# Performance work log

Measured on AMD Instinct MI355X. Metric: run time of the kernel, lower is better.

The kernel has to match this reference:

```python
import jax, jax.numpy as jnp
import numpy as np
import math

B, LQ, LK = 1024, 1, 1024
LQD, SQD, H = 256, 128, 2
HD = SQD // H  # 64
EPS = 1e-6


def _ln(x, g, b):
    mu = x.mean(-1, keepdims=True)
    var = ((x - mu) ** 2).mean(-1, keepdims=True)
    return (x - mu) / jnp.sqrt(var + EPS) * g + b


def setup_inputs() -> dict:
    key = jax.random.key(0)
    ks = jax.random.split(key, 16)
    w = lambda k, s: jax.random.normal(k, s, jnp.float32) * 0.02
    return {
        "q_feats": jax.random.normal(ks[0], (B, LQ, LQD), jnp.float32),
        "k_feats": jax.random.normal(ks[1], (B, LK, SQD), jnp.float32),
        "msk": jax.random.randint(ks[2], (B, LK), 0, 2).astype(jnp.int32),
        "ln1_g": jnp.ones(LQD), "ln1_b": jnp.zeros(LQD),
        "W1": w(ks[3], (LQD, SQD)), "b1": jnp.zeros(SQD),
        "lnq_g": jnp.ones(SQD), "lnq_b": jnp.zeros(SQD),
        "lnk_g": jnp.ones(SQD), "lnk_b": jnp.zeros(SQD),
        "Wq": w(ks[4], (SQD, SQD)), "bq": jnp.zeros(SQD),
        "Wk": w(ks[5], (SQD, SQD)), "bk": jnp.zeros(SQD),
        "Wv": w(ks[6], (SQD, SQD)), "bv": jnp.zeros(SQD),
        "Wo": w(ks[7], (SQD, SQD)), "bo": jnp.zeros(SQD),
        "scale_w": jax.random.uniform(ks[8], (SQD,), jnp.float32, 0.01, 2.0),
        "ln2_g": jnp.ones(SQD), "ln2_b": jnp.zeros(SQD),
        "W2": w(ks[9], (SQD, LQD)), "b2": jnp.zeros(LQD),
    }


def reference(q_feats, k_feats, msk, ln1_g, ln1_b, W1, b1, lnq_g, lnq_b,
              lnk_g, lnk_b, Wq, bq, Wk, bk, Wv, bv, Wo, bo, scale_w,
              ln2_g, ln2_b, W2, b2):
    gelu = lambda x: jax.nn.gelu(x, approximate=False)
    # q_block1: LN -> Linear -> GELU (dropout = identity in eval)
    q_atten = gelu(_ln(q_feats, ln1_g, ln1_b) @ W1 + b1)  # [B,LQ,SQD]
    kv_in = _ln(k_feats, lnk_g, lnk_b)                     # [B,LK,SQD]
    q_in = _ln(q_atten, lnq_g, lnq_b)
    # masked self-attention
    qh = (q_in @ Wq + bq).reshape(B, LQ, H, HD).transpose(0, 2, 1, 3)
    kh = (kv_in @ Wk + bk).reshape(B, LK, H, HD).transpose(0, 2, 1, 3)
    vh = (kv_in @ Wv + bv).reshape(B, LK, H, HD).transpose(0, 2, 1, 3)
    scores = jnp.einsum('bhqd,bhkd->bhqk', qh, kh) / math.sqrt(HD)
    m = msk.astype(scores.dtype)[:, None, None, :]  # [B,1,1,LK]
    scores = jnp.where(m == 0, -1e9, scores * m)
    attn = jax.nn.softmax(scores, axis=-1)
    ctx = jnp.einsum('bhqk,bhkd->bhqd', attn, vh)
    ctx = ctx.transpose(0, 2, 1, 3).reshape(B, LQ, SQD)
    attn_out = gelu(ctx @ Wo + bo)
    q_atten = q_atten + attn_out
    # scaled broadcast residual into k_feats
    scaled = jnp.swapaxes(q_atten * scale_w, 0, 1)         # [LQ,B,SQD]
    k_out = k_feats + jnp.tile(scaled, (B, 1, 1))          # [B,B,SQD]
    # q_block2
    q_out = q_feats + gelu(_ln(q_atten, ln2_g, ln2_b) @ W2 + b2)
    return (q_out, k_out)
```

## Files before the change

kernel.cpp:

```cpp
#include <hip/hip_runtime.h>
#include <math.h>

#define B_    1024
#define LK_   1024
#define LQD_  256
#define SQD_  128
#define EPSLN 1e-6f
#define LOG2E 1.4426950408889634f

#define TROWS 16
#define TF4   33
#define WREGF4 (TROWS * TF4)
#define WREGF  (WREGF4 * 4)

typedef float floatx4 __attribute__((ext_vector_type(4)));

__device__ __forceinline__ float gelu_exact(float x) {
    return 0.5f * x * (1.0f + erff(x * 0.70710678118654752f));
}

__global__ __launch_bounds__(256, 4)
void fused_joint_kernel(
    const float* __restrict__ q_feats, const float* __restrict__ k_feats,
    const int*   __restrict__ msk,
    const float* __restrict__ ln1_g, const float* __restrict__ ln1_b,
    const float* __restrict__ W1,    const float* __restrict__ b1,
    const float* __restrict__ lnq_g, const float* __restrict__ lnq_b,
    const float* __restrict__ lnk_g, const float* __restrict__ lnk_b,
    const float* __restrict__ Wq,    const float* __restrict__ bq,
    const float* __restrict__ Wk,    const float* __restrict__ bk,
    const float* __restrict__ Wv,    const float* __restrict__ bv,
    const float* __restrict__ Wo,    const float* __restrict__ bo,
    const float* __restrict__ scale_w,
    const float* __restrict__ ln2_g, const float* __restrict__ ln2_b,
    const float* __restrict__ W2,    const float* __restrict__ b2,
    float* __restrict__ q_out, float* __restrict__ k_out)
{
    const int b    = blockIdx.x;
    const int tid  = threadIdx.x;
    const int wave = tid >> 6;
    const int lane = tid & 63;

    __shared__ float4 s_tile4[4 * WREGF4];
    __shared__ float4 s_meta[4][TROWS];
    __shared__ unsigned short s_idxm[4][256];
    __shared__ __align__(16) float s_gu[2][128];
    __shared__ float s_q1[128];
    __shared__ float s_sc[128];
    __shared__ float s_red[8];
    __shared__ float s_ml[4][2][2];

    float* s_flat = (float*)s_tile4;
    float* s_qn = s_flat;
    float* s_qi = s_flat + 256;
    float* s_qh = s_flat + 384;
    float* s_u0 = s_flat + 512;
    float* s_u1 = s_flat + 640;
    float* s_c2 = s_flat + 768;
    float* s_wn  = s_flat + 1024;
    float* s_ctx = s_flat + 1280;
    float* s_qa  = s_flat + 1408;
    float* s_qn2 = s_flat + 1536;

    float x = q_feats[b * LQD_ + tid];
    float rs = x, rss = x * x;
    #pragma unroll
    for (int o = 32; o >= 1; o >>= 1) { rs += __shfl_xor(rs, o); rss += __shfl_xor(rss, o); }
    if (lane == 0) { s_red[wave * 2] = rs; s_red[wave * 2 + 1] = rss; }
    __syncthreads();
    {
        float sum  = s_red[0] + s_red[2] + s_red[4] + s_red[6];
        float ssum = s_red[1] + s_red[3] + s_red[5] + s_red[7];
        float mu   = sum * (1.0f / 256.0f);
        float var  = ssum * (1.0f / 256.0f) - mu * mu;
        float rstd = rsqrtf(var + EPSLN);
        s_qn[tid] = (x - mu) * rstd * ln1_g[tid] + ln1_b[tid];
    }
    __syncthreads();

    if (tid < 128) {
        float acc = b1[tid];
        #pragma unroll 4
        for (int c = 0; c < 256; ++c) acc = fmaf(s_qn[c], W1[c * 128 + tid], acc);
        s_q1[tid] = gelu_exact(acc);
    }
    __syncthreads();

    float v1 = (tid < 128) ? s_q1[tid] : 0.0f;
    rs = v1; rss = v1 * v1;
    #pragma unroll
    for (int o = 32; o >= 1; o >>= 1) { rs += __shfl_xor(rs, o); rss += __shfl_xor(rss, o); }
    __syncthreads();
    if (lane == 0) { s_red[wave * 2] = rs; s_red[wave * 2 + 1] = rss; }
    __syncthreads();
    {
        float sum  = s_red[0] + s_red[2] + s_red[4] + s_red[6];
        float ssum = s_red[1] + s_red[3] + s_red[5] + s_red[7];
        float mu   = sum * (1.0f / 128.0f);
        float var  = ssum * (1.0f / 128.0f) - mu * mu;
        float rstd = rsqrtf(var + EPSLN);
        if (tid < 128) s_qi[tid] = (v1 - mu) * rstd * lnq_g[tid] + lnq_b[tid];
    }
    __syncthreads();

    if (tid < 128) {
        float acc = bq[tid];
        #pragma unroll 4
        for (int c = 0; c < 128; ++c) acc = fmaf(s_qi[c], Wq[c * 128 + tid], acc);
        s_qh[tid] = acc;
    }
    __syncthreads();

    const float SCL = 0.125f * LOG2E;
    if (tid < 128) {
        float a0 = 0.f, a1 = 0.f;
        #pragma unroll 4
        for (int e = 0; e < 64; ++e) {
            a0 = fmaf(Wk[tid * 128 + e],      s_qh[e],      a0);
            a1 = fmaf(Wk[tid * 128 + 64 + e], s_qh[64 + e], a1);
        }
        s_u0[tid] = a0 * SCL;
        s_u1[tid] = a1 * SCL;
    }
    if (tid == 0) { float a = 0.f; for (int e = 0; e < 64; ++e) a = fmaf(bk[e],      s_qh[e],      a); s_c2[0] = a * SCL; }
    if (tid == 1) { float a = 0.f; for (int e = 0; e < 64; ++e) a = fmaf(bk[64 + e], s_qh[64 + e], a); s_c2[1] = a * SCL; }
    __syncthreads();

    const int  c0i = lane * 2, c1i = lane * 2 + 1;
    const float g0  = lnk_g[c0i], g1  = lnk_g[c1i];
    const float hb0 = lnk_b[c0i], hb1 = lnk_b[c1i];
    const float u00 = s_u0[c0i], u01 = s_u0[c1i];
    const float u10 = s_u1[c0i], u11 = s_u1[c1i];
    const float cc0 = s_c2[0],   cc1 = s_c2[1];
    if (tid < 128) {
        float g = lnk_g[tid];
        s_gu[0][tid] = s_u0[tid] * g;
        s_gu[1][tid] = s_u1[tid] * g;
    }
    float sgu0 = fmaf(g0, u00, g1 * u01);
    float sgu1 = fmaf(g0, u10, g1 * u11);
    float dd0  = fmaf(hb0, u00, hb1 * u01);
    float dd1  = fmaf(hb0, u10, hb1 * u11);
    #pragma unroll
    for (int o = 32; o >= 1; o >>= 1) {
        sgu0 += __shfl_xor(sgu0, o); sgu1 += __shfl_xor(sgu1, o);
        dd0  += __shfl_xor(dd0,  o); dd1  += __shfl_xor(dd1,  o);
    }
    const float d0 = dd0 + cc0, d1 = dd1 + cc1;

    const int* mrow = msk + b * LK_;
    int cnt = 0;
    #pragma unroll
    for (int i = 0; i < 4; ++i) {
        int r = (wave << 8) + (i << 6) + lane;
        int mk = mrow[r];
        unsigned long long bal = __ballot(mk != 0);
        int pre = __popcll(bal & ((1ull << lane) - 1ull));
        if (mk) s_idxm[wave][cnt + pre] = (unsigned short)r;
        cnt += __popcll(bal);
    }
    __syncthreads();

    float4* twave = s_tile4 + wave * WREGF4;
    const float* twf = (const float*)twave;
    const float4* kf4 = (const float4*)k_feats + (size_t)b * (LK_ * 32);
    const float4* gu04 = (const float4*)s_gu[0];
    const float4* gu14 = (const float4*)s_gu[1];
    const int half  = lane >> 5;
    const int chunk = lane & 31;
    const int arow  = lane & 15;
    const int aq    = lane >> 4;

    float m0 = -1e30f, l0 = 0.f, w00 = 0.f, w01 = 0.f;
    float m1 = -1e30f, l1 = 0.f, w10 = 0.f, w11 = 0.f;

    const int ntile = (cnt + TROWS - 1) / TROWS;
    float4 r0v, r1v, r2v, r3v, r4v, r5v, r6v, r7v;
    const float4 z4 = make_float4(0.f, 0.f, 0.f, 0.f);

    #define LOADT(base)                                                        \
    {                                                                          \
        int j_, gi_;                                                           \
        j_ = (base) + 0  + half; gi_ = (j_ < cnt) ? (int)s_idxm[wave][j_] : -1; \
        r0v = (gi_ >= 0) ? kf4[gi_ * 32 + chunk] : z4;                         \
        j_ = (base) + 2  + half; gi_ = (j_ < cnt) ? (int)s_idxm[wave][j_] : -1; \
        r1v = (gi_ >= 0) ? kf4[gi_ * 32 + chunk] : z4;                         \
        j_ = (base) + 4  + half; gi_ = (j_ < cnt) ? (int)s_idxm[wave][j_] : -1; \
        r2v = (gi_ >= 0) ? kf4[gi_ * 32 + chunk] : z4;                         \
        j_ = (base) + 6  + half; gi_ = (j_ < cnt) ? (int)s_idxm[wave][j_] : -1; \
        r3v = (gi_ >= 0) ? kf4[gi_ * 32 + chunk] : z4;                         \
        j_ = (base) + 8  + half; gi_ = (j_ < cnt) ? (int)s_idxm[wave][j_] : -1; \
        r4v = (gi_ >= 0) ? kf4[gi_ * 32 + chunk] : z4;                         \
        j_ = (base) + 10 + half; gi_ = (j_ < cnt) ? (int)s_idxm[wave][j_] : -1; \
        r5v = (gi_ >= 0) ? kf4[gi_ * 32 + chunk] : z4;                         \
        j_ = (base) + 12 + half; gi_ = (j_ < cnt) ? (int)s_idxm[wave][j_] : -1; \
        r6v = (gi_ >= 0) ? kf4[gi_ * 32 + chunk] : z4;                         \
        j_ = (base) + 14 + half; gi_ = (j_ < cnt) ? (int)s_idxm[wave][j_] : -1; \
        r7v = (gi_ >= 0) ? kf4[gi_ * 32 + chunk] : z4;                         \
    }

    if (ntile > 0) LOADT(0);

    for (int t = 0; t < ntile; ++t) {
        twave[(0  + half) * TF4 + chunk] = r0v;
        twave[(2  + half) * TF4 + chunk] = r1v;
        twave[(4  + half) * TF4 + chunk] = r2v;
        twave[(6  + half) * TF4 + chunk] = r3v;
        twave[(8  + half) * TF4 + chunk] = r4v;
        twave[(10 + half) * TF4 + chunk] = r5v;
        twave[(12 + half) * TF4 + chunk] = r6v;
        twave[(14 + half) * TF4 + chunk] = r7v;
        LOADT((t + 1) * TROWS);

        float sx = 0.f, sxx = 0.f, p0 = 0.f, p1 = 0.f;
        const float4* rowp = twave + arow * TF4 + aq * 8;
        #pragma unroll
        for (int k = 0; k < 8; ++k) {
            float4 v  = rowp[k];
            float4 ga = gu04[aq * 8 + k];
            float4 gb = gu14[aq * 8 + k];
            sx += (v.x + v.y) + (v.z + v.w);
            sxx = fmaf(v.x, v.x, fmaf(v.y, v.y, fmaf(v.z, v.z, fmaf(v.w, v.w, sxx))));
            p0  = fmaf(v.x, ga.x, fmaf(v.y, ga.y, fmaf(v.z, ga.z, fmaf(v.w, ga.w, p0))));
            p1  = fmaf(v.x, gb.x, fmaf(v.y, gb.y, fmaf(v.z, gb.z, fmaf(v.w, gb.w, p1))));
        }
        #pragma unroll
        for (int o = 16; o <= 32; o <<= 1) {
            sx += __shfl_xor(sx, o); sxx += __shfl_xor(sxx, o);
            p0 += __shfl_xor(p0, o); p1  += __shfl_xor(p1, o);
        }
        float mu   = sx * (1.f / 128.f);
        float var  = sxx * (1.f / 128.f) - mu * mu;
        float rstd = rsqrtf(var + EPSLN);
        bool  vrow = (t * TROWS + arow) < cnt;
        float sc0  = vrow ? fmaf(rstd, p0 - mu * sgu0, d0) : -1e30f;
        float sc1  = vrow ? fmaf(rstd, p1 - mu * sgu1, d1) : -1e30f;
        if (aq == 0) s_meta[wave][arow] = make_float4(sc0, sc1, mu, rstd);
        float t0 = sc0, t1 = sc1;
        #pragma unroll
        for (int o = 1; o <= 8; o <<= 1) {
            t0 = fmaxf(t0, __shfl_xor(t0, o));
            t1 = fmaxf(t1, __shfl_xor(t1, o));
        }
        float mn0 = fmaxf(m0, t0);
        float cr0 = exp2f(m0 - mn0);
        m0 = mn0; l0 *= cr0; w00 *= cr0; w01 *= cr0;
        float mn1 = fmaxf(m1, t1);
        float cr1 = exp2f(m1 - mn1);
        m1 = mn1; l1 *= cr1; w10 *= cr1; w11 *= cr1;

        #pragma unroll 4
        for (int j = 0; j < TROWS; ++j) {
            float4 mt = s_meta[wave][j];
            float2 xv = *(const float2*)(twf + j * 132 + 2 * lane);
            float pp0 = exp2f(mt.x - m0);
            float pp1 = exp2f(mt.y - m1);
            float xn0 = (xv.x - mt.z) * mt.w;
            float xn1 = (xv.y - mt.z) * mt.w;
            float kv0 = fmaf(xn0, g0, hb0);
            float kv1 = fmaf(xn1, g1, hb1);
            w00 = fmaf(pp0, kv0, w00); w01 = fmaf(pp0, kv1, w01);
            w10 = fmaf(pp1, kv0, w10); w11 = fmaf(pp1, kv1, w11);
            l0 += pp0; l1 += pp1;
        }
    }
    #undef LOADT

    {
        float* myreg = s_flat + wave * WREGF;
        myreg[c0i] = w00; myreg[c1i] = w01;
        myreg[128 + c0i] = w10; myreg[128 + c1i] = w11;
        if (lane == 0) {
            s_ml[wave][0][0] = m0; s_ml[wave][0][1] = l0;
            s_ml[wave][1][0] = m1; s_ml[wave][1][1] = l1;
        }
    }
    __syncthreads();

    if (tid < 128) {
        #pragma unroll
        for (int h = 0; h < 2; ++h) {
            float mg = fmaxf(fmaxf(s_ml[0][h][0], s_ml[1][h][0]),
                             fmaxf(s_ml[2][h][0], s_ml[3][h][0]));
            float lt = 0.f, wt = 0.f;
            #pragma unroll
            for (int wv = 0; wv < 4; ++wv) {
                float e = exp2f(s_ml[wv][h][0] - mg);
                lt += s_ml[wv][h][1] * e;
                wt += s_flat[wv * WREGF + h * 128 + tid] * e;
            }
            s_wn[h * 128 + tid] = wt / lt;
        }
    }
    __syncthreads();

    if (tid < 128) {
        int h = tid >> 6;
        float acc = bv[tid];
        #pragma unroll 4
        for (int c = 0; c < 128; ++c) acc = fmaf(s_wn[h * 128 + c], Wv[c * 128 + tid], acc);
        s_ctx[tid] = acc;
    }
    __syncthreads();

    if (tid < 128) {
        float acc = bo[tid];
        #pragma unroll 4
        for (int c = 0; c < 128; ++c) acc = fmaf(s_ctx[c], Wo[c * 128 + tid], acc);
        float qa = s_q1[tid] + gelu_exact(acc);
        s_qa[tid] = qa;
        s_sc[tid] = qa * scale_w[tid];
    }
    __syncthreads();

    float v2 = (tid < 128) ? s_qa[tid] : 0.0f;
    rs = v2; rss = v2 * v2;
    #pragma unroll
    for (int o = 32; o >= 1; o >>= 1) { rs += __shfl_xor(rs, o); rss += __shfl_xor(rss, o); }
    __syncthreads();
    if (lane == 0) { s_red[wave * 2] = rs; s_red[wave * 2 + 1] = rss; }
    __syncthreads();
    {
        float sum  = s_red[0] + s_red[2] + s_red[4] + s_red[6];
        float ssum = s_red[1] + s_red[3] + s_red[5] + s_red[7];
        float mu   = sum * (1.0f / 128.0f);
        float var  = ssum * (1.0f / 128.0f) - mu * mu;
        float rstd = rsqrtf(var + EPSLN);
        if (tid < 128) s_qn2[tid] = (v2 - mu) * rstd * ln2_g[tid] + ln2_b[tid];
    }
    __syncthreads();

    {
        float acc = b2[tid];
        #pragma unroll 4
        for (int c = 0; c < 128; ++c) acc = fmaf(s_qn2[c], W2[c * 256 + tid], acc);
        q_out[b * LQD_ + tid] = q_feats[b * LQD_ + tid] + gelu_exact(acc);
    }

    {
        const int c4 = tid & 31;
        const int rr = tid >> 5;
        const float4 sv = ((const float4*)s_sc)[c4];
        const size_t colbase = (size_t)b * 32 + c4;
        const floatx4* __restrict__ kin4  = (const floatx4*)k_feats;
        floatx4*       __restrict__ kout4 = (floatx4*)k_out;
        #pragma unroll 4
        for (int b2 = rr; b2 < B_; b2 += 8) {
            size_t o = (size_t)b2 * (LK_ * 32) + colbase;
            floatx4 kx = kin4[o];
            floatx4 ov;
            ov.x = kx.x + sv.x; ov.y = kx.y + sv.y;
            ov.z = kx.z + sv.z; ov.w = kx.w + sv.w;
            __builtin_nontemporal_store(ov, &kout4[o]);
        }
    }
}

extern "C" void kernel_launch(void* const* d_in, const int* in_sizes, int n_in,
                              void* d_out, int out_size, void* d_ws, size_t ws_size,
                              hipStream_t stream)
{
    (void)in_sizes; (void)n_in; (void)out_size; (void)d_ws; (void)ws_size;
    const float* q_feats = (const float*)d_in[0];
    const float* k_feats = (const float*)d_in[1];
    const int*   msk     = (const int*)d_in[2];
    const float* ln1_g   = (const float*)d_in[3];
    const float* ln1_b   = (const float*)d_in[4];
    const float* W1      = (const float*)d_in[5];
    const float* b1      = (const float*)d_in[6];
    const float* lnq_g   = (const float*)d_in[7];
    const float* lnq_b   = (const float*)d_in[8];
    const float* lnk_g   = (const float*)d_in[9];
    const float* lnk_b   = (const float*)d_in[10];
    const float* Wq      = (const float*)d_in[11];
    const float* bq      = (const float*)d_in[12];
    const float* Wk      = (const float*)d_in[13];
    const float* bk      = (const float*)d_in[14];
    const float* Wv      = (const float*)d_in[15];
    const float* bv      = (const float*)d_in[16];
    const float* Wo      = (const float*)d_in[17];
    const float* bo      = (const float*)d_in[18];
    const float* scale_w = (const float*)d_in[19];
    const float* ln2_g   = (const float*)d_in[20];
    const float* ln2_b   = (const float*)d_in[21];
    const float* W2      = (const float*)d_in[22];
    const float* b2      = (const float*)d_in[23];

    float* q_out = (float*)d_out;
    float* k_out = (float*)d_out + (size_t)B_ * LQD_;

    fused_joint_kernel<<<B_, 256, 0, stream>>>(
        q_feats, k_feats, msk, ln1_g, ln1_b, W1, b1, lnq_g, lnq_b,
        lnk_g, lnk_b, Wq, bq, Wk, bk, Wv, bv, Wo, bo, scale_w,
        ln2_g, ln2_b, W2, b2, q_out, k_out);
}
```

Before: 400.3 us.

## Split k_out broadcast-add into a separate grid-stride streaming kernel

Moves the large k_out = k_feats + scaled broadcast out of the fused per-batch attention kernel. The attention kernel now writes the scaled vector to workspace, and a second kernel streams k_feats to k_out with contiguous, coalesced float4 accesses across a grid-stride loop. The old path had each block touch strided columns across all rows, which gives poor access locality. The split costs an extra launch and a workspace round trip, and it drops the nontemporal store hint.

```diff
diff --git a/kernel.cpp b/kernel.cpp
--- a/kernel.cpp
+++ b/kernel.cpp
@@ -20,7 +20,7 @@
 }
 
 __global__ __launch_bounds__(256, 4)
-void fused_joint_kernel(
+void fused_q_attn_kernel(
     const float* __restrict__ q_feats, const float* __restrict__ k_feats,
     const int*   __restrict__ msk,
     const float* __restrict__ ln1_g, const float* __restrict__ ln1_b,
@@ -34,7 +34,7 @@
     const float* __restrict__ scale_w,
     const float* __restrict__ ln2_g, const float* __restrict__ ln2_b,
     const float* __restrict__ W2,    const float* __restrict__ b2,
-    float* __restrict__ q_out, float* __restrict__ k_out)
+    float* __restrict__ q_out, float* __restrict__ sc_ws)
 {
     const int b    = blockIdx.x;
     const int tid  = threadIdx.x;
@@ -46,7 +46,6 @@
     __shared__ unsigned short s_idxm[4][256];
     __shared__ __align__(16) float s_gu[2][128];
     __shared__ float s_q1[128];
-    __shared__ float s_sc[128];
     __shared__ float s_red[8];
     __shared__ float s_ml[4][2][2];
 
@@ -309,7 +308,7 @@
         for (int c = 0; c < 128; ++c) acc = fmaf(s_ctx[c], Wo[c * 128 + tid], acc);
         float qa = s_q1[tid] + gelu_exact(acc);
         s_qa[tid] = qa;
-        s_sc[tid] = qa * scale_w[tid];
+        sc_ws[b * 128 + tid] = qa * scale_w[tid];
     }
     __syncthreads();
 
@@ -336,23 +335,21 @@
         for (int c = 0; c < 128; ++c) acc = fmaf(s_qn2[c], W2[c * 256 + tid], acc);
         q_out[b * LQD_ + tid] = q_feats[b * LQD_ + tid] + gelu_exact(acc);
     }
-
-    {
-        const int c4 = tid & 31;
-        const int rr = tid >> 5;
-        const float4 sv = ((const float4*)s_sc)[c4];
-        const size_t colbase = (size_t)b * 32 + c4;
-        const floatx4* __restrict__ kin4  = (const floatx4*)k_feats;
-        floatx4*       __restrict__ kout4 = (floatx4*)k_out;
-        #pragma unroll 4
-        for (int b2 = rr; b2 < B_; b2 += 8) {
-            size_t o = (size_t)b2 * (LK_ * 32) + colbase;
-            floatx4 kx = kin4[o];
-            floatx4 ov;
-            ov.x = kx.x + sv.x; ov.y = kx.y + sv.y;
-            ov.z = kx.z + sv.z; ov.w = kx.w + sv.w;
-            __builtin_nontemporal_store(ov, &kout4[o]);
-        }
+}
+
+__global__ __launch_bounds__(256)
+void kout_stream_kernel(const floatx4* __restrict__ kf,
+                        const floatx4* __restrict__ sc,
+                        floatx4* __restrict__ out)
+{
+    const int total4 = B_ * LK_ * (SQD_ / 4);
+    const int stride = gridDim.x * blockDim.x;
+    int idx = blockIdx.x * blockDim.x + threadIdx.x;
+    #pragma unroll 8
+    for (; idx < total4; idx += stride) {
+        floatx4 k = kf[idx];
+        floatx4 s = sc[idx & 32767];
+        out[idx] = k + s;
     }
 }
 
@@ -360,7 +357,7 @@
                               void* d_out, int out_size, void* d_ws, size_t ws_size,
                               hipStream_t stream)
 {
-    (void)in_sizes; (void)n_in; (void)out_size; (void)d_ws; (void)ws_size;
+    (void)in_sizes; (void)n_in; (void)out_size; (void)ws_size;
     const float* q_feats = (const float*)d_in[0];
     const float* k_feats = (const float*)d_in[1];
     const int*   msk     = (const int*)d_in[2];
@@ -388,9 +385,13 @@
 
     float* q_out = (float*)d_out;
     float* k_out = (float*)d_out + (size_t)B_ * LQD_;
-
-    fused_joint_kernel<<<B_, 256, 0, stream>>>(
+    float* sc_ws = (float*)d_ws;
+
+    fused_q_attn_kernel<<<B_, 256, 0, stream>>>(
         q_feats, k_feats, msk, ln1_g, ln1_b, W1, b1, lnq_g, lnq_b,
         lnk_g, lnk_b, Wq, bq, Wk, bk, Wv, bv, Wo, bo, scale_w,
-        ln2_g, ln2_b, W2, b2, q_out, k_out);
+        ln2_g, ln2_b, W2, b2, q_out, sc_ws);
+
+    kout_stream_kernel<<<2048, 256, 0, stream>>>(
+        (const floatx4*)k_feats, (const floatx4*)sc_ws, (floatx4*)k_out);
 }
```

Result: slower. 431.1 us (+7.7%).

## Replace masked-row compaction with dense tile loads and additive mask bias

Applied to the files above, without the earlier changes.

Removes the ballot-based compaction of unmasked key rows and instead streams all 256 rows per wave contiguously, applying the mask as a -1e30 score bias read from a shared byte array. The aim is simpler, fully coalesced, predictable loads without index indirection. In exchange, roughly twice as many key rows are read and normalized. The broadcast residual write also switches from nontemporal stores to regular stores, which may raise cache pollution.

```diff
diff --git a/kernel.cpp b/kernel.cpp
--- a/kernel.cpp
+++ b/kernel.cpp
@@ -12,8 +12,6 @@
 #define TF4   33
 #define WREGF4 (TROWS * TF4)
 #define WREGF  (WREGF4 * 4)
-
-typedef float floatx4 __attribute__((ext_vector_type(4)));
 
 __device__ __forceinline__ float gelu_exact(float x) {
     return 0.5f * x * (1.0f + erff(x * 0.70710678118654752f));
@@ -43,7 +41,7 @@
 
     __shared__ float4 s_tile4[4 * WREGF4];
     __shared__ float4 s_meta[4][TROWS];
-    __shared__ unsigned short s_idxm[4][256];
+    __shared__ unsigned char s_mskf[1024];
     __shared__ __align__(16) float s_gu[2][128];
     __shared__ float s_q1[128];
     __shared__ float s_sc[128];
@@ -62,6 +60,14 @@
     float* s_qa  = s_flat + 1408;
     float* s_qn2 = s_flat + 1536;
 
+    {
+        int4 mv = ((const int4*)(msk + b * LK_))[tid];
+        s_mskf[tid * 4 + 0] = (unsigned char)(mv.x != 0);
+        s_mskf[tid * 4 + 1] = (unsigned char)(mv.y != 0);
+        s_mskf[tid * 4 + 2] = (unsigned char)(mv.z != 0);
+        s_mskf[tid * 4 + 3] = (unsigned char)(mv.w != 0);
+    }
+
     float x = q_feats[b * LQD_ + tid];
     float rs = x, rss = x * x;
     #pragma unroll
@@ -147,23 +153,11 @@
         dd0  += __shfl_xor(dd0,  o); dd1  += __shfl_xor(dd1,  o);
     }
     const float d0 = dd0 + cc0, d1 = dd1 + cc1;
-
-    const int* mrow = msk + b * LK_;
-    int cnt = 0;
-    #pragma unroll
-    for (int i = 0; i < 4; ++i) {
-        int r = (wave << 8) + (i << 6) + lane;
-        int mk = mrow[r];
-        unsigned long long bal = __ballot(mk != 0);
-        int pre = __popcll(bal & ((1ull << lane) - 1ull));
-        if (mk) s_idxm[wave][cnt + pre] = (unsigned short)r;
-        cnt += __popcll(bal);
-    }
     __syncthreads();
 
     float4* twave = s_tile4 + wave * WREGF4;
     const float* twf = (const float*)twave;
-    const float4* kf4 = (const float4*)k_feats + (size_t)b * (LK_ * 32);
+    const float4* kf4 = (const float4*)k_feats + (size_t)b * (LK_ * 32) + (wave << 8) * 32;
     const float4* gu04 = (const float4*)s_gu[0];
     const float4* gu14 = (const float4*)s_gu[1];
     const int half  = lane >> 5;
@@ -174,34 +168,24 @@
     float m0 = -1e30f, l0 = 0.f, w00 = 0.f, w01 = 0.f;
     float m1 = -1e30f, l1 = 0.f, w10 = 0.f, w11 = 0.f;
 
-    const int ntile = (cnt + TROWS - 1) / TROWS;
     float4 r0v, r1v, r2v, r3v, r4v, r5v, r6v, r7v;
-    const float4 z4 = make_float4(0.f, 0.f, 0.f, 0.f);
-
-    #define LOADT(base)                                                        \
-    {                                                                          \
-        int j_, gi_;                                                           \
-        j_ = (base) + 0  + half; gi_ = (j_ < cnt) ? (int)s_idxm[wave][j_] : -1; \
-        r0v = (gi_ >= 0) ? kf4[gi_ * 32 + chunk] : z4;                         \
-        j_ = (base) + 2  + half; gi_ = (j_ < cnt) ? (int)s_idxm[wave][j_] : -1; \
-        r1v = (gi_ >= 0) ? kf4[gi_ * 32 + chunk] : z4;                         \
-        j_ = (base) + 4  + half; gi_ = (j_ < cnt) ? (int)s_idxm[wave][j_] : -1; \
-        r2v = (gi_ >= 0) ? kf4[gi_ * 32 + chunk] : z4;                         \
-        j_ = (base) + 6  + half; gi_ = (j_ < cnt) ? (int)s_idxm[wave][j_] : -1; \
-        r3v = (gi_ >= 0) ? kf4[gi_ * 32 + chunk] : z4;                         \
-        j_ = (base) + 8  + half; gi_ = (j_ < cnt) ? (int)s_idxm[wave][j_] : -1; \
-        r4v = (gi_ >= 0) ? kf4[gi_ * 32 + chunk] : z4;                         \
-        j_ = (base) + 10 + half; gi_ = (j_ < cnt) ? (int)s_idxm[wave][j_] : -1; \
-        r5v = (gi_ >= 0) ? kf4[gi_ * 32 + chunk] : z4;                         \
-        j_ = (base) + 12 + half; gi_ = (j_ < cnt) ? (int)s_idxm[wave][j_] : -1; \
-        r6v = (gi_ >= 0) ? kf4[gi_ * 32 + chunk] : z4;                         \
-        j_ = (base) + 14 + half; gi_ = (j_ < cnt) ? (int)s_idxm[wave][j_] : -1; \
-        r7v = (gi_ >= 0) ? kf4[gi_ * 32 + chunk] : z4;                         \
-    }
-
-    if (ntile > 0) LOADT(0);
-
-    for (int t = 0; t < ntile; ++t) {
+
+    #define LOADT(base)                                   \
+    {                                                     \
+        const float4* p_ = kf4 + ((base) + half) * 32 + chunk; \
+        r0v = p_[0 * 32];                                 \
+        r1v = p_[2 * 32];                                 \
+        r2v = p_[4 * 32];                                 \
+        r3v = p_[6 * 32];                                 \
+        r4v = p_[8 * 32];                                 \
+        r5v = p_[10 * 32];                                \
+        r6v = p_[12 * 32];                                \
+        r7v = p_[14 * 32];                                \
+    }
+
+    LOADT(0);
+
+    for (int t = 0; t < 16; ++t) {
         twave[(0  + half) * TF4 + chunk] = r0v;
         twave[(2  + half) * TF4 + chunk] = r1v;
         twave[(4  + half) * TF4 + chunk] = r2v;
@@ -210,7 +194,10 @@
         twave[(10 + half) * TF4 + chunk] = r5v;
         twave[(12 + half) * TF4 + chunk] = r6v;
         twave[(14 + half) * TF4 + chunk] = r7v;
-        LOADT((t + 1) * TROWS);
+        {
+            int nb = (t + 1) * TROWS;
+            LOADT(nb > 240 ? 240 : nb);
+        }
 
         float sx = 0.f, sxx = 0.f, p0 = 0.f, p1 = 0.f;
         const float4* rowp = twave + arow * TF4 + aq * 8;
@@ -232,9 +219,9 @@
         float mu   = sx * (1.f / 128.f);
         float var  = sxx * (1.f / 128.f) - mu * mu;
         float rstd = rsqrtf(var + EPSLN);
-        bool  vrow = (t * TROWS + arow) < cnt;
-        float sc0  = vrow ? fmaf(rstd, p0 - mu * sgu0, d0) : -1e30f;
-        float sc1  = vrow ? fmaf(rstd, p1 - mu * sgu1, d1) : -1e30f;
+        float bias = s_mskf[(wave << 8) + t * TROWS + arow] ? 0.f : -1e30f;
+        float sc0  = fmaf(rstd, p0 - mu * sgu0, d0) + bias;
+        float sc1  = fmaf(rstd, p1 - mu * sgu1, d1) + bias;
         if (aq == 0) s_meta[wave][arow] = make_float4(sc0, sc1, mu, rstd);
         float t0 = sc0, t1 = sc1;
         #pragma unroll
@@ -342,16 +329,14 @@
         const int rr = tid >> 5;
         const float4 sv = ((const float4*)s_sc)[c4];
         const size_t colbase = (size_t)b * 32 + c4;
-        const floatx4* __restrict__ kin4  = (const floatx4*)k_feats;
-        floatx4*       __restrict__ kout4 = (floatx4*)k_out;
+        const float4* __restrict__ kin4  = (const float4*)k_feats;
+        float4*       __restrict__ kout4 = (float4*)k_out;
         #pragma unroll 4
         for (int b2 = rr; b2 < B_; b2 += 8) {
             size_t o = (size_t)b2 * (LK_ * 32) + colbase;
-            floatx4 kx = kin4[o];
-            floatx4 ov;
-            ov.x = kx.x + sv.x; ov.y = kx.y + sv.y;
-            ov.z = kx.z + sv.z; ov.w = kx.w + sv.w;
-            __builtin_nontemporal_store(ov, &kout4[o]);
+            float4 kx = kin4[o];
+            float4 ov = make_float4(kx.x + sv.x, kx.y + sv.y, kx.z + sv.z, kx.w + sv.w);
+            kout4[o] = ov;
         }
     }
 }
```

Result: slower. 454.3 us (+13.5%).
